# Kernel tuning notes

Hardware: AMD Instinct MI355X
Metric: run time of the kernel (lower is better)

The kernel has to match this reference:

```python
import jax, jax.numpy as jnp
import numpy as np

D = 1024; H = 16; K = 64; BK = 32; FFN = 4096; LORA = 48; CHUNK = 64
THETA_CLIP = float(np.pi / 2)
THETA_INIT = float(np.pi / 16)


def layernorm(x, g, b, eps=1e-6):
    m = x.mean(-1, keepdims=True)
    v = ((x - m) ** 2).mean(-1, keepdims=True)
    return (x - m) * jax.lax.rsqrt(v + eps) * g + b


def setup_inputs() -> dict:
    key = jax.random.key(0)
    ks = jax.random.split(key, 24)
    w = lambda k, s: jax.random.normal(k, s, jnp.float32) * 0.02
    return {
        "x": jax.random.normal(ks[0], (4, 2048, D), jnp.float32),
        "Wq": w(ks[1], (D, D)), "bq": jnp.zeros((D,), jnp.float32),
        "Wk": w(ks[2], (D, D)), "bk": jnp.zeros((D,), jnp.float32),
        "Wv": w(ks[3], (D, D)), "bv": jnp.zeros((D,), jnp.float32),
        "Wo": w(ks[4], (D, D)), "bo": jnp.zeros((D,), jnp.float32),
        "n1g": jnp.ones((D,), jnp.float32), "n1b": jnp.zeros((D,), jnp.float32),
        "n2g": jnp.ones((D,), jnp.float32), "n2b": jnp.zeros((D,), jnp.float32),
        "theta_base": jax.random.uniform(ks[5], (H, BK), jnp.float32, -THETA_INIT, THETA_INIT),
        "theta_w1": w(ks[6], (D, LORA)),
        "theta_w2": jax.random.uniform(ks[7], (LORA, H * BK), jnp.float32, -0.01, 0.01),
        "lambda_base": jax.random.uniform(ks[8], (H, BK), jnp.float32, 0.5, 6.0),
        "eta": jax.random.normal(ks[9], (H, BK), jnp.float32) * 0.1,
        "Wf1": w(ks[10], (D, FFN)), "bf1": jnp.zeros((FFN,), jnp.float32),
        "Wf2": w(ks[11], (FFN, D)), "bf2": jnp.zeros((D,), jnp.float32),
    }


def _forward(x, Wq, bq, Wk, bk, Wv, bv, Wo, bo, n1g, n1b, n2g, n2b,
             theta_base, theta_w1, theta_w2, lambda_base, eta, Wf1, bf1, Wf2, bf2):
    B, T, _ = x.shape
    NC = T // CHUNK
    xn = layernorm(x, n1g, n1b)
    # projections -> (B, H, T, K)
    q = (xn @ Wq + bq).reshape(B, T, H, K).transpose(0, 2, 1, 3)
    k = (xn @ Wk + bk).reshape(B, T, H, K).transpose(0, 2, 1, 3)
    v = (xn @ Wv + bv).reshape(B, T, H, K).transpose(0, 2, 1, 3)
    phi_k = jnp.where(k > 0, k + 1.0, jnp.exp(k))  # elu(k) + 1
    qp = q.reshape(B, H, T, BK, 2)
    kp = phi_k.reshape(B, H, T, BK, 2)
    q_c = jax.lax.complex(qp[..., 0], qp[..., 1])  # (B,H,T,BK) complex64
    k_c = jax.lax.complex(kp[..., 0], kp[..., 1])
    # data-dependent rotation angles via LoRA
    lora = jnp.tanh(xn @ theta_w1) @ theta_w2  # (B,T,H*BK)
    theta = theta_base[None, None] + lora.reshape(B, T, H, BK)
    theta = jnp.clip(theta, -THETA_CLIP, THETA_CLIP).transpose(0, 2, 1, 3)  # (B,H,T,BK)
    lam = lambda_base[None, :, None, :] + eta[None, :, None, :] * theta ** 2
    log_z = jax.lax.complex(-lam, theta)  # complex log-decay per step

    def chunks(a):  # (B,H,T,...) -> (NC,B,H,CHUNK,...)
        return jnp.moveaxis(a.reshape(B, H, NC, CHUNK, *a.shape[3:]), 2, 0)

    tril = jnp.tril(jnp.ones((CHUNK, CHUNK), bool))[None, None, :, :, None]

    def step(c, inputs):
        lz, kc, qc, vf = inputs  # (B,H,tc,BK)x3, (B,H,tc,K)
        cumlog = jnp.cumsum(lz, axis=2)
        diff = cumlog[:, :, :, None, :] - cumlog[:, :, None, :, :]  # (B,H,tc,tc,BK)
        real = jnp.where(tril, diff.real, -60.0)
        A = jnp.where(tril, jnp.exp(jax.lax.complex(real, diff.imag)),
                      jnp.zeros((), jnp.complex64))
        scaled_k = A * kc[:, :, None, :, :]
        S_intra = jnp.einsum('bhtsk,bhsv->bhtkv', scaled_k, vf.astype(jnp.complex64))
        decay = jnp.exp(cumlog)
        S_total = decay[..., None] * c[:, :, None] + S_intra  # (B,H,tc,BK,K)
        y = jnp.einsum('bhtk,bhtkv->bhtv', jnp.conj(qc), S_total).real
        return S_total[:, :, -1], y

    c0 = jnp.zeros((B, H, BK, K), jnp.complex64)
    _, ys = jax.lax.scan(step, c0, (chunks(log_z), chunks(k_c), chunks(q_c), chunks(v)))
    out = jnp.moveaxis(ys, 0, 2).reshape(B, H, T, K)
    attn = out.transpose(0, 2, 1, 3).reshape(B, T, D) @ Wo + bo
    x1 = x + attn
    h = layernorm(x1, n2g, n2b)
    return x1 + jax.nn.gelu(h @ Wf1 + bf1) @ Wf2 + bf2


def reference(x, Wq, bq, Wk, bk, Wv, bv, Wo, bo, n1g, n1b, n2g, n2b,
              theta_base, theta_w1, theta_w2, lambda_base, eta, Wf1, bf1, Wf2, bf2):
    return _forward(x, Wq, bq, Wk, bk, Wv, bv, Wo, bo, n1g, n1b, n2g, n2b,
                    theta_base, theta_w1, theta_w2, lambda_base, eta, Wf1, bf1, Wf2, bf2)
```

## Files before the change

### kernel.cpp

```cpp
#include <hip/hip_runtime.h>


typedef __bf16 bf16x8 __attribute__((ext_vector_type(8)));
typedef float f32x4 __attribute__((ext_vector_type(4)));

__device__ __forceinline__ unsigned short f2bf(float f) {
  unsigned int u = __builtin_bit_cast(unsigned int, f);
  u += 0x7FFFu + ((u >> 16) & 1u);
  return (unsigned short)(u >> 16);
}
__device__ __forceinline__ float bf2f(unsigned short u) {
  unsigned int x = ((unsigned int)u) << 16;
  return __builtin_bit_cast(float, x);
}
__device__ __forceinline__ unsigned int pack2(float a, float b) {
  return (unsigned int)f2bf(a) | ((unsigned int)f2bf(b) << 16);
}

__device__ __forceinline__ void gload_lds16(const void* g, void* l) {
  __builtin_amdgcn_global_load_lds((const __attribute__((address_space(1))) void*)g,
                                   (__attribute__((address_space(3))) void*)l, 16, 0, 0);
}

__device__ __forceinline__ float gelu_tanh(float v) {
  const float z = 0.7978845608028654f * fmaf(0.044715f * v * v, v, v);
  const float e = __expf(2.f * z);
  return 0.5f * v * (2.f - 2.f / (1.f + e));
}

__global__ void fill_kernel(float* p, float v, int n) {
  int i = blockIdx.x * 256 + threadIdx.x;
  if (i < n) p[i] = v;
}

__global__ __launch_bounds__(256) void ln_kernel(
    const float* __restrict__ x, const float* __restrict__ g,
    const float* __restrict__ b, unsigned short* __restrict__ out) {
  const int row = blockIdx.x, tid = threadIdx.x;
  float4 v = ((const float4*)(x + (size_t)row * 1024))[tid];
  float s = v.x + v.y + v.z + v.w;
  float sq = v.x * v.x + v.y * v.y + v.z * v.z + v.w * v.w;
#pragma unroll
  for (int o = 32; o > 0; o >>= 1) { s += __shfl_xor(s, o); sq += __shfl_xor(sq, o); }
  __shared__ float red[8];
  const int wid = tid >> 6;
  if ((tid & 63) == 0) { red[wid] = s; red[4 + wid] = sq; }
  __syncthreads();
  s = red[0] + red[1] + red[2] + red[3];
  sq = red[4] + red[5] + red[6] + red[7];
  const float mean = s * (1.f / 1024.f);
  const float var = sq * (1.f / 1024.f) - mean * mean;
  const float rstd = rsqrtf(var + 1e-6f);
  float4 gv = ((const float4*)g)[tid];
  float4 bvv = ((const float4*)b)[tid];
  ushort4 o4;
  o4.x = f2bf((v.x - mean) * rstd * gv.x + bvv.x);
  o4.y = f2bf((v.y - mean) * rstd * gv.y + bvv.y);
  o4.z = f2bf((v.z - mean) * rstd * gv.z + bvv.z);
  o4.w = f2bf((v.w - mean) * rstd * gv.w + bvv.w);
  *(ushort4*)(out + (size_t)row * 1024 + tid * 4) = o4;
}

__global__ __launch_bounds__(256) void transpose_bf16(
    const float* __restrict__ src, unsigned short* __restrict__ dst, int K, int N) {
  __shared__ float tile[32][33];
  const int n0 = blockIdx.x * 32, k0 = blockIdx.y * 32;
  const int tx = threadIdx.x, ty = threadIdx.y;
#pragma unroll
  for (int j = 0; j < 32; j += 8) tile[tx][ty + j] = src[(size_t)(k0 + ty + j) * N + n0 + tx];
  __syncthreads();
#pragma unroll
  for (int j = 0; j < 32; j += 8)
    dst[(size_t)(n0 + ty + j) * K + k0 + tx] = f2bf(tile[ty + j][tx]);
}

__global__ __launch_bounds__(256) void prep_wcat(
    const float* __restrict__ Wq, const float* __restrict__ Wk,
    const float* __restrict__ Wv, const float* __restrict__ tw1,
    unsigned short* __restrict__ dst) {
  __shared__ float tile[32][33];
  const int r0 = blockIdx.x * 32, c0 = blockIdx.y * 32;
  const int tx = threadIdx.x, ty = threadIdx.y;
  const int r = r0 + tx;
#pragma unroll
  for (int j = 0; j < 32; j += 8) {
    const int c = c0 + ty + j;
    float v;
    if (r < 1024) v = Wq[(size_t)c * 1024 + r];
    else if (r < 2048) v = Wk[(size_t)c * 1024 + (r - 1024)];
    else if (r < 3072) v = Wv[(size_t)c * 1024 + (r - 2048)];
    else if (r < 3120) v = tw1[(size_t)c * 48 + (r - 3072)];
    else v = 0.f;
    tile[tx][ty + j] = v;
  }
  __syncthreads();
#pragma unroll
  for (int j = 0; j < 32; j += 8)
    dst[(size_t)(r0 + ty + j) * 1024 + c0 + tx] = f2bf(tile[ty + j][tx]);
}

__global__ void biascat_kernel(const float* bq, const float* bk, const float* bv, float* dst) {
  int i = blockIdx.x * 256 + threadIdx.x;
  if (i >= 3200) return;
  float v = 0.f;
  if (i < 1024) v = bq[i];
  else if (i < 2048) v = bk[i - 1024];
  else if (i < 3072) v = bv[i - 2048];
  dst[i] = v;
}

template <int MODE>
__global__ __launch_bounds__(256) void gemm_kernel(
    const unsigned short* __restrict__ A, const unsigned short* __restrict__ BT,
    const float* __restrict__ bias, const float* __restrict__ res,
    void* __restrict__ out, int N, int Kd) {
  __shared__ unsigned short As[128 * 64];
  __shared__ unsigned short Bs[128 * 64];
  const int nwg = gridDim.x * gridDim.y;
  int d = blockIdx.y * gridDim.x + blockIdx.x;
  d = (d & 7) * (nwg >> 3) + (d >> 3);
  const int n0 = (d % gridDim.x) * 128, m0 = (d / gridDim.x) * 128;

  const int tid = threadIdx.x, wv = tid >> 6, ln = tid & 63;
  const int wm = wv >> 1, wn = wv & 1;
  const int l15 = ln & 15, hi4 = ln >> 4;
  const int rbase = wv * 8 + (ln >> 3);
  const int kgofs = ((ln & 7) ^ ((ln >> 3) & 7)) * 8;

  f32x4 acc[4][4] = {};
  for (int k0 = 0; k0 < Kd; k0 += 64) {
#pragma unroll
    for (int jj = 0; jj < 4; ++jj) {
      gload_lds16(A + (size_t)(m0 + jj * 32 + rbase) * Kd + k0 + kgofs,
                  (char*)As + (jj * 256 + wv * 64) * 16);
      gload_lds16(BT + (size_t)(n0 + jj * 32 + rbase) * Kd + k0 + kgofs,
                  (char*)Bs + (jj * 256 + wv * 64) * 16);
    }
    __syncthreads();
#pragma unroll
    for (int kk = 0; kk < 64; kk += 32) {
      const int kg = (kk >> 3) + hi4;
      bf16x8 av[4], bv[4];
#pragma unroll
      for (int f = 0; f < 4; ++f) {
        const int ra = wm * 64 + f * 16 + l15;
        const int rb2 = wn * 64 + f * 16 + l15;
        av[f] = *(const bf16x8*)&As[(ra * 8 + (kg ^ (ra & 7))) * 8];
        bv[f] = *(const bf16x8*)&Bs[(rb2 * 8 + (kg ^ (rb2 & 7))) * 8];
      }
#pragma unroll
      for (int fm = 0; fm < 4; ++fm)
#pragma unroll
        for (int fn = 0; fn < 4; ++fn)
          acc[fm][fn] = __builtin_amdgcn_mfma_f32_16x16x32_bf16(av[fm], bv[fn], acc[fm][fn], 0, 0, 0);
    }
    __syncthreads();
  }
  const int rb = hi4 * 4;
#pragma unroll
  for (int fm = 0; fm < 4; ++fm) {
#pragma unroll
    for (int fn = 0; fn < 4; ++fn) {
      const int row = m0 + wm * 64 + fm * 16 + rb;
      const int col = n0 + wn * 64 + fn * 16 + l15;
      const float bval = bias[col];
#pragma unroll
      for (int r = 0; r < 4; ++r) {
        float v = acc[fm][fn][r] + bval;
        const size_t oi = (size_t)(row + r) * N + col;
        if constexpr (MODE == 1) v += res[oi];
        if constexpr (MODE == 2) {
          ((unsigned short*)out)[oi] = f2bf(gelu_tanh(v));
        } else if constexpr (MODE == 3) {
          ((unsigned short*)out)[oi] = f2bf(v);
        } else {
          ((float*)out)[oi] = v;
        }
      }
    }
  }
}

__global__ __launch_bounds__(256) void lora2_kernel(
    const unsigned short* __restrict__ qkv, const float* __restrict__ w2,
    const float* __restrict__ tbase, float* __restrict__ theta) {
  __shared__ float lt[8][48];
  const int m0 = blockIdx.x * 32;
  const int tid = threadIdx.x;
  const int col = tid * 2;
  const float tb0 = tbase[col], tb1 = tbase[col + 1];
  for (int grp = 0; grp < 4; ++grp) {
    const int mg = m0 + grp * 8;
    __syncthreads();
    for (int idx = tid; idx < 384; idx += 256) {
      const int tok = idx / 48, jj = idx % 48;
      lt[tok][jj] = tanhf(bf2f(qkv[(size_t)(mg + tok) * 3200 + 3072 + jj]));
    }
    __syncthreads();
    float a0[8], a1[8];
#pragma unroll
    for (int tok = 0; tok < 8; ++tok) { a0[tok] = tb0; a1[tok] = tb1; }
    for (int jj = 0; jj < 48; ++jj) {
      const float2 w = *(const float2*)&w2[(size_t)jj * 512 + col];
#pragma unroll
      for (int tok = 0; tok < 8; ++tok) {
        const float l = lt[tok][jj];
        a0[tok] = fmaf(l, w.x, a0[tok]);
        a1[tok] = fmaf(l, w.y, a1[tok]);
      }
    }
    const float CL = 1.5707963267948966f;
#pragma unroll
    for (int tok = 0; tok < 8; ++tok) {
      float c0 = fminf(fmaxf(a0[tok], -CL), CL);
      float c1 = fminf(fmaxf(a1[tok], -CL), CL);
      *(float2*)&theta[(size_t)(mg + tok) * 512 + col] = make_float2(c0, c1);
    }
  }
}

__global__ __launch_bounds__(256) void attn_intra(
    const unsigned short* __restrict__ qkv, const float* __restrict__ theta,
    const float* __restrict__ lamb, const float* __restrict__ eta,
    float* __restrict__ yi, unsigned short* __restrict__ QG,
    unsigned short* __restrict__ TCG, float* __restrict__ Dg) {
  const int c = blockIdx.x, bh = blockIdx.y;
  const int b = bh >> 4, h = bh & 15;
  const int tid = threadIdx.x, wv = tid >> 6, lane = tid & 63;
  const int sc = c * 4 + wv;
  const int cid = bh * 128 + sc;
  const int mw = b * 2048 + sc * 16;

  __shared__ unsigned short QDm[4][16][64];
  __shared__ unsigned short KDm[4][16][64];
  __shared__ unsigned short KdET[4][64][32];
  __shared__ unsigned short VT[4][64][32];
  __shared__ unsigned short Gs[4][16][32];

  {
    unsigned int* kz = (unsigned int*)&KdET[wv][0][0];
    unsigned int* vz = (unsigned int*)&VT[wv][0][0];
    for (int idx = lane; idx < 512; idx += 64) {
      const int r = idx >> 3, p = (idx & 7) + 8;
      kz[r * 16 + p] = 0; vz[r * 16 + p] = 0;
    }
    unsigned int* gz = (unsigned int*)&Gs[wv][0][0];
    for (int idx = lane; idx < 128; idx += 64) {
      const int r = idx >> 3, p = (idx & 7) + 8;
      gz[r * 16 + p] = 0;
    }
  }
  for (int ss = 0; ss < 16; ++ss)
    VT[wv][lane][ss] = qkv[(size_t)(mw + ss) * 3200 + 2048 + h * 64 + lane];

  const int bk = lane & 31, th = lane >> 5;
  const float lb = lamb[h * 32 + bk], et = eta[h * 32 + bk];
  float L[8], Th[8], qr[8], qi[8], kr[8], ki[8];
  float runL = 0.f, runT = 0.f;
#pragma unroll
  for (int i = 0; i < 8; ++i) {
    const size_t m = (size_t)(mw + th * 8 + i);
    const float tv = theta[m * 512 + h * 32 + bk];
    const float lam = fmaf(et * tv, tv, lb);
    runL += lam; L[i] = runL;
    runT += tv;  Th[i] = runT;
    const unsigned int qp = *(const unsigned int*)&qkv[m * 3200 + h * 64 + 2 * bk];
    const unsigned int kp = *(const unsigned int*)&qkv[m * 3200 + 1024 + h * 64 + 2 * bk];
    qr[i] = bf2f((unsigned short)(qp & 0xFFFF)); qi[i] = bf2f((unsigned short)(qp >> 16));
    const float kx = bf2f((unsigned short)(kp & 0xFFFF));
    const float ky = bf2f((unsigned short)(kp >> 16));
    kr[i] = kx > 0.f ? kx + 1.f : __expf(kx);
    ki[i] = ky > 0.f ? ky + 1.f : __expf(ky);
  }
  const float oL = __shfl_xor(runL, 32), oT = __shfl_xor(runT, 32);
  const float Lm = th ? oL : runL;
  const float Tm = th ? oT : runT;
  const float Ltot = runL + oL, Ttot = runT + oT;
  const float Lbase = th ? oL : 0.f, Tbase = th ? oT : 0.f;
  float Es, Ec; __sincosf(Tm, &Es, &Ec);
  const float Ee = __expf(-Lm);
  const float Er = Ee * Ec, Ei = Ee * Es;
  float Fs, Fc; __sincosf(Ttot - Tm, &Fs, &Fc);
  const float Fe = __expf(-(Ltot - Lm));
  const float Fr = Fe * Fc, Fi = Fe * Fs;
  if (th == 0) {
    float Ds, Dc; __sincosf(Ttot, &Ds, &Dc);
    const float De = __expf(-Ltot);
    *(float2*)&Dg[((size_t)cid * 32 + bk) * 2] = make_float2(De * Dc, De * Ds);
  }
  unsigned int* qd32 = (unsigned int*)&QDm[wv][0][0];
  unsigned int* kd32 = (unsigned int*)&KDm[wv][0][0];
#pragma unroll
  for (int i = 0; i < 8; ++i) {
    const int t = th * 8 + i;
    const float Lg = Lbase + L[i], Tg = Tbase + Th[i];
    const float dm = __expf(-(Lg - Lm));
    float sn, cs; __sincosf(Tg - Tm, &sn, &cs);
    const float qmr = dm * (qr[i] * cs + qi[i] * sn);
    const float qmi = dm * (qr[i] * sn - qi[i] * cs);
    const float rd = 1.f / dm;
    const float kmr = rd * (kr[i] * cs + ki[i] * sn);
    const float kmi = rd * (ki[i] * cs - kr[i] * sn);
    const int sidx = (t * 32 + bk) ^ ((t & 7) << 2);
    qd32[sidx] = pack2(qmr, qmi);
    kd32[sidx] = pack2(kmr, -kmi);
    ((unsigned int*)QG)[(size_t)cid * 512 + t * 32 + bk] =
        pack2(qmr * Er - qmi * Ei, qmr * Ei + qmi * Er);
    const float er = kmr * Fr - kmi * Fi;
    const float ei = kmr * Fi + kmi * Fr;
    KdET[wv][bk][t] = f2bf(er);
    KdET[wv][32 + bk][t] = f2bf(ei);
  }

  const int l15 = lane & 15, hi = lane >> 4;
  const char* qb = (const char*)&QDm[wv][0][0];
  const char* kb = (const char*)&KDm[wv][0][0];
  f32x4 z = {};
  f32x4 g = z;
  {
    bf16x8 a0 = *(const bf16x8*)(qb + l15 * 128 + ((16 * hi) ^ ((l15 & 7) << 4)));
    bf16x8 b0 = *(const bf16x8*)(kb + l15 * 128 + ((16 * hi) ^ ((l15 & 7) << 4)));
    bf16x8 a1 = *(const bf16x8*)(qb + l15 * 128 + ((64 + 16 * hi) ^ ((l15 & 7) << 4)));
    bf16x8 b1 = *(const bf16x8*)(kb + l15 * 128 + ((64 + 16 * hi) ^ ((l15 & 7) << 4)));
    g = __builtin_amdgcn_mfma_f32_16x16x32_bf16(a0, b0, g, 0, 0, 0);
    g = __builtin_amdgcn_mfma_f32_16x16x32_bf16(a1, b1, g, 0, 0, 0);
  }
#pragma unroll
  for (int r = 0; r < 4; ++r) {
    const float gv = (l15 <= 4 * hi + r) ? g[r] : 0.f;
    Gs[wv][4 * hi + r][l15] = f2bf(gv);
  }
  const char* gsb = (const char*)&Gs[wv][0][0];
  const char* vtb = (const char*)&VT[wv][0][0];
  bf16x8 aG = *(const bf16x8*)(gsb + l15 * 64 + 16 * hi);
#pragma unroll
  for (int nt = 0; nt < 4; ++nt) {
    bf16x8 bV = *(const bf16x8*)(vtb + (nt * 16 + l15) * 64 + 16 * hi);
    f32x4 y = __builtin_amdgcn_mfma_f32_16x16x32_bf16(aG, bV, z, 0, 0, 0);
#pragma unroll
    for (int r = 0; r < 4; ++r)
      yi[(size_t)cid * 1024 + (4 * hi + r) * 64 + nt * 16 + l15] = y[r];
  }
  const char* keb = (const char*)&KdET[wv][0][0];
#pragma unroll
  for (int mt = 0; mt < 4; ++mt) {
    bf16x8 aT = *(const bf16x8*)(keb + (mt * 16 + l15) * 64 + 16 * hi);
#pragma unroll
    for (int nt = 0; nt < 4; ++nt) {
      bf16x8 bV = *(const bf16x8*)(vtb + (nt * 16 + l15) * 64 + 16 * hi);
      f32x4 t4 = __builtin_amdgcn_mfma_f32_16x16x32_bf16(aT, bV, z, 0, 0, 0);
#pragma unroll
      for (int r = 0; r < 4; ++r)
        TCG[(size_t)cid * 4096 + (mt * 16 + 4 * hi + r) * 64 + nt * 16 + l15] = f2bf(t4[r]);
    }
  }
}

__global__ __launch_bounds__(256) void scanB_kernel(
    const unsigned short* __restrict__ TCG, const float* __restrict__ Dg,
    unsigned int* __restrict__ CPACK) {
  const int bh = blockIdx.x & 63, g = blockIdx.x >> 6;
  const int tid = threadIdx.x;
  const int v = g * 8 + (tid >> 5), bk = tid & 31;
  const size_t base = (size_t)bh * 128;
  float Cr = 0.f, Ci = 0.f;
  float trx[4], tix[4]; float2 dx[4];
  auto LOADQ = [&](int c0, float* tr, float* ti, float2* dd) {
#pragma unroll
    for (int u = 0; u < 4; ++u) {
      const size_t cid = base + c0 + u;
      tr[u] = bf2f(TCG[cid * 4096 + bk * 64 + v]);
      ti[u] = bf2f(TCG[cid * 4096 + (32 + bk) * 64 + v]);
      dd[u] = *(const float2*)&Dg[(cid * 32 + bk) * 2];
    }
  };
  LOADQ(0, trx, tix, dx);
  for (int c0 = 0; c0 < 128; c0 += 4) {
    float tra[4], tia[4]; float2 da[4];
#pragma unroll
    for (int u = 0; u < 4; ++u) { tra[u] = trx[u]; tia[u] = tix[u]; da[u] = dx[u]; }
    if (c0 + 4 < 128) LOADQ(c0 + 4, trx, tix, dx);
#pragma unroll
    for (int u = 0; u < 4; ++u) {
      CPACK[(base + c0 + u) * 2048 + v * 32 + bk] = pack2(Cr, -Ci);
      const float nr = fmaf(da[u].x, Cr, fmaf(-da[u].y, Ci, tra[u]));
      const float ni = fmaf(da[u].x, Ci, fmaf(da[u].y, Cr, tia[u]));
      Cr = nr; Ci = ni;
    }
  }
}

__global__ __launch_bounds__(256) void attn_cross(
    const float* __restrict__ yi, const unsigned short* __restrict__ QG,
    const unsigned int* __restrict__ CPACK, unsigned short* __restrict__ attn) {
  const int c = blockIdx.x, bh = blockIdx.y;
  const int b = bh >> 4, h = bh & 15;
  const int tid = threadIdx.x, wv = tid >> 6, lane = tid & 63;
  const int sc = c * 4 + wv, cid = bh * 128 + sc;
  const int mw = b * 2048 + sc * 16;
  __shared__ unsigned short Cp[4][64][64];
  __shared__ unsigned short Qs[4][16][64];
  unsigned int* cp32 = (unsigned int*)&Cp[wv][0][0];
  const unsigned int* cg = CPACK + (size_t)cid * 2048;
  for (int ii = 0; ii < 32; ++ii) {
    const int flat = ii * 64 + lane;
    const int row = flat >> 5, col = flat & 31;
    cp32[(row * 32 + col) ^ ((row & 7) << 2)] = cg[flat];
  }
  unsigned int* qs32 = (unsigned int*)&Qs[wv][0][0];
  const unsigned int* qg = (const unsigned int*)QG + (size_t)cid * 512;
  for (int ii = 0; ii < 8; ++ii) {
    const int flat = ii * 64 + lane;
    const int row = flat >> 5, col = flat & 31;
    qs32[(row * 32 + col) ^ ((row & 7) << 2)] = qg[flat];
  }
  const int l15 = lane & 15, hi = lane >> 4;
  const char* qb = (const char*)&Qs[wv][0][0];
  const char* cb = (const char*)&Cp[wv][0][0];
  bf16x8 a0 = *(const bf16x8*)(qb + l15 * 128 + ((16 * hi) ^ ((l15 & 7) << 4)));
  bf16x8 a1 = *(const bf16x8*)(qb + l15 * 128 + ((64 + 16 * hi) ^ ((l15 & 7) << 4)));
  f32x4 z = {};
#pragma unroll
  for (int nt = 0; nt < 4; ++nt) {
    const int vr = nt * 16 + l15;
    bf16x8 b0 = *(const bf16x8*)(cb + vr * 128 + ((16 * hi) ^ ((vr & 7) << 4)));
    bf16x8 b1 = *(const bf16x8*)(cb + vr * 128 + ((64 + 16 * hi) ^ ((vr & 7) << 4)));
    f32x4 y = __builtin_amdgcn_mfma_f32_16x16x32_bf16(a0, b0, z, 0, 0, 0);
    y = __builtin_amdgcn_mfma_f32_16x16x32_bf16(a1, b1, y, 0, 0, 0);
#pragma unroll
    for (int r = 0; r < 4; ++r) {
      const int t = 4 * hi + r;
      const float out = y[r] + yi[(size_t)cid * 1024 + t * 64 + vr];
      attn[(size_t)(mw + t) * 1024 + h * 64 + vr] = f2bf(out);
    }
  }
}

extern "C" void kernel_launch(void* const* d_in, const int* in_sizes, int n_in,
                              void* d_out, int out_size, void* d_ws, size_t ws_size,
                              hipStream_t stream) {
  const float* x   = (const float*)d_in[0];
  const float* Wq  = (const float*)d_in[1];
  const float* bq  = (const float*)d_in[2];
  const float* Wk  = (const float*)d_in[3];
  const float* bk_ = (const float*)d_in[4];
  const float* Wv  = (const float*)d_in[5];
  const float* bv  = (const float*)d_in[6];
  const float* Wo  = (const float*)d_in[7];
  const float* bo  = (const float*)d_in[8];
  const float* n1g = (const float*)d_in[9];
  const float* n1b = (const float*)d_in[10];
  const float* n2g = (const float*)d_in[11];
  const float* n2b = (const float*)d_in[12];
  const float* thb = (const float*)d_in[13];
  const float* tw1 = (const float*)d_in[14];
  const float* tw2 = (const float*)d_in[15];
  const float* lamb= (const float*)d_in[16];
  const float* eta = (const float*)d_in[17];
  const float* Wf1 = (const float*)d_in[18];
  const float* bf1 = (const float*)d_in[19];
  const float* Wf2 = (const float*)d_in[20];
  const float* bf2 = (const float*)d_in[21];

  char* ws = (char*)d_ws;
  size_t off = 0;
  auto alloc = [&](size_t bytes) {
    size_t r = off;
    off += (bytes + 255) & ~(size_t)255;
    return r;
  };
  unsigned short* WCAT = (unsigned short*)(ws + alloc(3200ull * 1024 * 2));
  unsigned short* WOT  = (unsigned short*)(ws + alloc(1024ull * 1024 * 2));
  unsigned short* WF1T = (unsigned short*)(ws + alloc(4096ull * 1024 * 2));
  unsigned short* WF2T = (unsigned short*)(ws + alloc(1024ull * 4096 * 2));
  float* BIASC = (float*)(ws + alloc(3200ull * 4));
  unsigned short* XN = (unsigned short*)(ws + alloc(8192ull * 1024 * 2));
  char* QKVbase = ws + alloc(8192ull * 4096 * 2);
  unsigned short* QKV = (unsigned short*)QKVbase;
  unsigned int* CPACK = (unsigned int*)QKVbase;
  unsigned short* GBUF = (unsigned short*)QKVbase;
  float* THETA = (float*)(ws + alloc(8192ull * 512 * 4));
  unsigned short* ATTN = (unsigned short*)THETA;
  float* YI = (float*)(ws + alloc(8192ull * 1024 * 4));
  float* X1 = YI;
  unsigned short* QG = (unsigned short*)(ws + alloc(8192ull * 1024 * 2));
  unsigned short* TCG = (unsigned short*)(ws + alloc(8192ull * 4096 * 2));
  float* DG = (float*)(ws + alloc(8192ull * 32 * 2 * 4));

  if (ws_size < off) {
    fill_kernel<<<dim3((out_size + 255) / 256), dim3(256), 0, stream>>>((float*)d_out, 12345.0f, out_size);
    return;
  }

  const dim3 b256(256), b32x8(32, 8);

  prep_wcat<<<dim3(100, 32), b32x8, 0, stream>>>(Wq, Wk, Wv, tw1, WCAT);
  transpose_bf16<<<dim3(32, 32), b32x8, 0, stream>>>(Wo, WOT, 1024, 1024);
  transpose_bf16<<<dim3(128, 32), b32x8, 0, stream>>>(Wf1, WF1T, 1024, 4096);
  transpose_bf16<<<dim3(32, 128), b32x8, 0, stream>>>(Wf2, WF2T, 4096, 1024);
  biascat_kernel<<<dim3(13), b256, 0, stream>>>(bq, bk_, bv, BIASC);

  ln_kernel<<<dim3(8192), b256, 0, stream>>>(x, n1g, n1b, XN);
  gemm_kernel<3><<<dim3(25, 64), b256, 0, stream>>>(XN, WCAT, BIASC, nullptr, QKV, 3200, 1024);
  lora2_kernel<<<dim3(256), b256, 0, stream>>>(QKV, tw2, thb, THETA);
  attn_intra<<<dim3(32, 64), b256, 0, stream>>>(QKV, THETA, lamb, eta, YI, QG, TCG, DG);
  scanB_kernel<<<dim3(512), b256, 0, stream>>>(TCG, DG, CPACK);
  attn_cross<<<dim3(32, 64), b256, 0, stream>>>(YI, QG, CPACK, ATTN);
  gemm_kernel<1><<<dim3(8, 64), b256, 0, stream>>>(ATTN, WOT, bo, x, X1, 1024, 1024);
  ln_kernel<<<dim3(8192), b256, 0, stream>>>(X1, n2g, n2b, XN);
  gemm_kernel<2><<<dim3(32, 64), b256, 0, stream>>>(XN, WF1T, bf1, nullptr, GBUF, 4096, 1024);
  gemm_kernel<1><<<dim3(8, 64), b256, 0, stream>>>(GBUF, WF2T, bf2, X1, d_out, 1024, 4096);
}
```

Measured before the change: 520.9 us.

## Replace GEMM with double-buffered 512-thread kernel, fuse prep launches, retile scan output layout

Swaps the single-buffered 128x128 GEMM for a 512-thread kernel that double-buffers A/B tiles in LDS with K-step 32, uses explicit vmcnt waits and barriers, raises MFMA priority, and optionally processes 256-row M tiles. The goal is to overlap global loads with MFMA work and get more reuse per block. It also merges the weight transpose and bias concat kernels into one launch, pads the QKV width to 3328, and changes the CPACK layout so scan writes and cross-attention reads are coalesced. The hand-written waitcnt pipeline is fragile, and the padding adds some wasted GEMM columns.

```diff
diff --git a/kernel.cpp b/kernel.cpp
--- a/kernel.cpp
+++ b/kernel.cpp
@@ -1,5 +1,7 @@
 #include <hip/hip_runtime.h>
 
+
+#define QS 3328
 
 typedef __bf16 bf16x8 __attribute__((ext_vector_type(8)));
 typedef float f32x4 __attribute__((ext_vector_type(4)));
@@ -61,11 +63,11 @@
   *(ushort4*)(out + (size_t)row * 1024 + tid * 4) = o4;
 }
 
-__global__ __launch_bounds__(256) void transpose_bf16(
-    const float* __restrict__ src, unsigned short* __restrict__ dst, int K, int N) {
+__device__ __forceinline__ void tr_tile(
+    const float* __restrict__ src, unsigned short* __restrict__ dst,
+    int K, int N, int bx, int by, int tx, int ty) {
   __shared__ float tile[32][33];
-  const int n0 = blockIdx.x * 32, k0 = blockIdx.y * 32;
-  const int tx = threadIdx.x, ty = threadIdx.y;
+  const int n0 = bx * 32, k0 = by * 32;
 #pragma unroll
   for (int j = 0; j < 32; j += 8) tile[tx][ty + j] = src[(size_t)(k0 + ty + j) * N + n0 + tx];
   __syncthreads();
@@ -74,107 +76,165 @@
     dst[(size_t)(n0 + ty + j) * K + k0 + tx] = f2bf(tile[ty + j][tx]);
 }
 
-__global__ __launch_bounds__(256) void prep_wcat(
+__global__ __launch_bounds__(256) void prep_all(
     const float* __restrict__ Wq, const float* __restrict__ Wk,
     const float* __restrict__ Wv, const float* __restrict__ tw1,
-    unsigned short* __restrict__ dst) {
-  __shared__ float tile[32][33];
-  const int r0 = blockIdx.x * 32, c0 = blockIdx.y * 32;
-  const int tx = threadIdx.x, ty = threadIdx.y;
-  const int r = r0 + tx;
-#pragma unroll
-  for (int j = 0; j < 32; j += 8) {
-    const int c = c0 + ty + j;
-    float v;
-    if (r < 1024) v = Wq[(size_t)c * 1024 + r];
-    else if (r < 2048) v = Wk[(size_t)c * 1024 + (r - 1024)];
-    else if (r < 3072) v = Wv[(size_t)c * 1024 + (r - 2048)];
-    else if (r < 3120) v = tw1[(size_t)c * 48 + (r - 3072)];
-    else v = 0.f;
-    tile[tx][ty + j] = v;
-  }
-  __syncthreads();
-#pragma unroll
-  for (int j = 0; j < 32; j += 8)
-    dst[(size_t)(r0 + ty + j) * 1024 + c0 + tx] = f2bf(tile[ty + j][tx]);
-}
-
-__global__ void biascat_kernel(const float* bq, const float* bk, const float* bv, float* dst) {
-  int i = blockIdx.x * 256 + threadIdx.x;
-  if (i >= 3200) return;
-  float v = 0.f;
-  if (i < 1024) v = bq[i];
-  else if (i < 2048) v = bk[i - 1024];
-  else if (i < 3072) v = bv[i - 2048];
-  dst[i] = v;
-}
-
-template <int MODE>
-__global__ __launch_bounds__(256) void gemm_kernel(
+    const float* __restrict__ Wo, const float* __restrict__ Wf1,
+    const float* __restrict__ Wf2,
+    const float* __restrict__ bq, const float* __restrict__ bk,
+    const float* __restrict__ bv,
+    unsigned short* __restrict__ WCAT, unsigned short* __restrict__ WOT,
+    unsigned short* __restrict__ WF1T, unsigned short* __restrict__ WF2T,
+    float* __restrict__ BIASC) {
+  const int id = blockIdx.x;
+  const int tx = threadIdx.x & 31, ty = threadIdx.x >> 5;
+  if (id < 3328) {
+    __shared__ float tile[32][33];
+    const int bx = id % 104, by = id / 104;
+    const int r0 = bx * 32, c0 = by * 32;
+    const int r = r0 + tx;
+#pragma unroll
+    for (int j = 0; j < 32; j += 8) {
+      const int c = c0 + ty + j;
+      float v;
+      if (r < 1024) v = Wq[(size_t)c * 1024 + r];
+      else if (r < 2048) v = Wk[(size_t)c * 1024 + (r - 1024)];
+      else if (r < 3072) v = Wv[(size_t)c * 1024 + (r - 2048)];
+      else if (r < 3120) v = tw1[(size_t)c * 48 + (r - 3072)];
+      else v = 0.f;
+      tile[tx][ty + j] = v;
+    }
+    __syncthreads();
+#pragma unroll
+    for (int j = 0; j < 32; j += 8)
+      WCAT[(size_t)(r0 + ty + j) * 1024 + c0 + tx] = f2bf(tile[ty + j][tx]);
+  } else if (id < 4352) {
+    const int i2 = id - 3328;
+    tr_tile(Wo, WOT, 1024, 1024, i2 % 32, i2 / 32, tx, ty);
+  } else if (id < 8448) {
+    const int i3 = id - 4352;
+    tr_tile(Wf1, WF1T, 1024, 4096, i3 % 128, i3 / 128, tx, ty);
+  } else if (id < 12544) {
+    const int i4 = id - 8448;
+    tr_tile(Wf2, WF2T, 4096, 1024, i4 % 32, i4 / 32, tx, ty);
+  } else {
+    const int i5 = (id - 12544) * 256 + threadIdx.x;
+    if (i5 < QS) {
+      float v = 0.f;
+      if (i5 < 1024) v = bq[i5];
+      else if (i5 < 2048) v = bk[i5 - 1024];
+      else if (i5 < 3072) v = bv[i5 - 2048];
+      BIASC[i5] = v;
+    }
+  }
+}
+
+template <int MODE, int MB>
+__global__ __launch_bounds__(512, 4) void gemmco_kernel(
     const unsigned short* __restrict__ A, const unsigned short* __restrict__ BT,
     const float* __restrict__ bias, const float* __restrict__ res,
-    void* __restrict__ out, int N, int Kd) {
-  __shared__ unsigned short As[128 * 64];
-  __shared__ unsigned short Bs[128 * 64];
+    void* __restrict__ out, int N, int Kstride, int Klen) {
+  constexpr int NR = (MB == 2) ? 4 : 2;
+  constexpr int ABUF = MB * 8192;
+  __shared__ __align__(16) char SA[2 * ABUF];
+  __shared__ __align__(16) char SB[2 * 8192];
+
   const int nwg = gridDim.x * gridDim.y;
   int d = blockIdx.y * gridDim.x + blockIdx.x;
   d = (d & 7) * (nwg >> 3) + (d >> 3);
-  const int n0 = (d % gridDim.x) * 128, m0 = (d / gridDim.x) * 128;
+  const int n0 = (d % gridDim.x) * 128, m0 = (d / gridDim.x) * (MB * 128);
 
   const int tid = threadIdx.x, wv = tid >> 6, ln = tid & 63;
-  const int wm = wv >> 1, wn = wv & 1;
-  const int l15 = ln & 15, hi4 = ln >> 4;
-  const int rbase = wv * 8 + (ln >> 3);
-  const int kgofs = ((ln & 7) ^ ((ln >> 3) & 7)) * 8;
-
-  f32x4 acc[4][4] = {};
-  for (int k0 = 0; k0 < Kd; k0 += 64) {
-#pragma unroll
-    for (int jj = 0; jj < 4; ++jj) {
-      gload_lds16(A + (size_t)(m0 + jj * 32 + rbase) * Kd + k0 + kgofs,
-                  (char*)As + (jj * 256 + wv * 64) * 16);
-      gload_lds16(BT + (size_t)(n0 + jj * 32 + rbase) * Kd + k0 + kgofs,
-                  (char*)Bs + (jj * 256 + wv * 64) * 16);
-    }
-    __syncthreads();
-#pragma unroll
-    for (int kk = 0; kk < 64; kk += 32) {
-      const int kg = (kk >> 3) + hi4;
-      bf16x8 av[4], bv[4];
-#pragma unroll
-      for (int f = 0; f < 4; ++f) {
-        const int ra = wm * 64 + f * 16 + l15;
-        const int rb2 = wn * 64 + f * 16 + l15;
-        av[f] = *(const bf16x8*)&As[(ra * 8 + (kg ^ (ra & 7))) * 8];
-        bv[f] = *(const bf16x8*)&Bs[(rb2 * 8 + (kg ^ (rb2 & 7))) * 8];
-      }
-#pragma unroll
-      for (int fm = 0; fm < 4; ++fm)
-#pragma unroll
-        for (int fn = 0; fn < 4; ++fn)
-          acc[fm][fn] = __builtin_amdgcn_mfma_f32_16x16x32_bf16(av[fm], bv[fn], acc[fm][fn], 0, 0, 0);
-    }
-    __syncthreads();
-  }
-  const int rb = hi4 * 4;
-#pragma unroll
-  for (int fm = 0; fm < 4; ++fm) {
-#pragma unroll
-    for (int fn = 0; fn < 4; ++fn) {
-      const int row = m0 + wm * 64 + fm * 16 + rb;
-      const int col = n0 + wn * 64 + fn * 16 + l15;
+  const int l15 = ln & 15, hi4 = (ln >> 4) & 3;
+  const int wm = (MB == 2) ? (wv >> 1) : (wv >> 2);
+  const int wncol = (MB == 2) ? (wv & 1) * 64 : (wv & 3) * 32;
+
+  const int srow = ln >> 2;
+  const int skg = (ln & 3) ^ ((ln >> 3) & 3);
+  const unsigned short* ga0 = A + (size_t)(m0 + wv * 16 + srow) * Kstride + skg * 8;
+  const unsigned short* ga1 = A + (size_t)(m0 + 128 + wv * 16 + srow) * Kstride + skg * 8;
+  const unsigned short* gb0 = BT + (size_t)(n0 + wv * 16 + srow) * Kstride + skg * 8;
+
+  auto STA = [&](int p) {
+    gload_lds16(ga0, SA + p * ABUF + wv * 1024);
+    ga0 += 32;
+    if constexpr (MB == 2) {
+      gload_lds16(ga1, SA + p * ABUF + 8192 + wv * 1024);
+      ga1 += 32;
+    }
+  };
+  auto STB = [&](int p) {
+    gload_lds16(gb0, SB + p * 8192 + wv * 1024);
+    gb0 += 32;
+  };
+
+  const int kch = (hi4 ^ ((l15 >> 1) & 3)) * 16;
+  const char* aA = SA + (wm * 64 + l15) * 64 + kch;
+  const char* aB = SB + (wncol + l15) * 64 + kch;
+
+  f32x4 acc[4][NR] = {};
+  const int nt = Klen >> 5;
+
+  STA(0);
+  STB(0);
+  STA(1);
+  if constexpr (MB == 2) asm volatile("s_waitcnt vmcnt(2)" ::: "memory");
+  else                   asm volatile("s_waitcnt vmcnt(1)" ::: "memory");
+  __builtin_amdgcn_s_barrier();
+
+#define GTILE(P, T)                                                            \
+  {                                                                            \
+    if ((T) + 1 < nt) STB((P) ^ 1);                                            \
+    bf16x8 bfr[NR];                                                            \
+    _Pragma("unroll")                                                          \
+    for (int nr = 0; nr < NR; ++nr)                                            \
+      bfr[nr] = *(const bf16x8*)(aB + (P) * 8192 + nr * 1024);                 \
+    _Pragma("unroll")                                                          \
+    for (int mr = 0; mr < 4; ++mr) {                                           \
+      bf16x8 af = *(const bf16x8*)(aA + (P) * ABUF + mr * 1024);               \
+      __builtin_amdgcn_s_setprio(1);                                           \
+      _Pragma("unroll")                                                        \
+      for (int nr = 0; nr < NR; ++nr)                                          \
+        acc[mr][nr] = __builtin_amdgcn_mfma_f32_16x16x32_bf16(af, bfr[nr],     \
+                                                              acc[mr][nr], 0, 0, 0); \
+      __builtin_amdgcn_s_setprio(0);                                           \
+    }                                                                          \
+    __builtin_amdgcn_s_barrier();                                              \
+    if ((T) + 2 < nt) STA(P);                                                  \
+    if ((T) + 1 < nt) {                                                        \
+      if ((T) + 2 < nt) {                                                      \
+        if constexpr (MB == 2) asm volatile("s_waitcnt vmcnt(2)" ::: "memory");\
+        else                   asm volatile("s_waitcnt vmcnt(1)" ::: "memory");\
+      } else {                                                                 \
+        asm volatile("s_waitcnt vmcnt(0)" ::: "memory");                       \
+      }                                                                        \
+      __builtin_amdgcn_s_barrier();                                            \
+    }                                                                          \
+  }
+
+  for (int t = 0; t < nt; t += 2) {
+    GTILE(0, t);
+    GTILE(1, t + 1);
+  }
+#undef GTILE
+
+#pragma unroll
+  for (int mr = 0; mr < 4; ++mr) {
+#pragma unroll
+    for (int nr = 0; nr < NR; ++nr) {
+      const int row = m0 + wm * 64 + mr * 16 + hi4 * 4;
+      const int col = n0 + wncol + nr * 16 + l15;
       const float bval = bias[col];
 #pragma unroll
       for (int r = 0; r < 4; ++r) {
-        float v = acc[fm][fn][r] + bval;
+        const float v = acc[mr][nr][r] + bval;
         const size_t oi = (size_t)(row + r) * N + col;
-        if constexpr (MODE == 1) v += res[oi];
-        if constexpr (MODE == 2) {
+        if constexpr (MODE == 1) {
+          ((float*)out)[oi] = v + res[oi];
+        } else if constexpr (MODE == 2) {
           ((unsigned short*)out)[oi] = f2bf(gelu_tanh(v));
-        } else if constexpr (MODE == 3) {
+        } else {
           ((unsigned short*)out)[oi] = f2bf(v);
-        } else {
-          ((float*)out)[oi] = v;
         }
       }
     }
@@ -194,7 +254,7 @@
     __syncthreads();
     for (int idx = tid; idx < 384; idx += 256) {
       const int tok = idx / 48, jj = idx % 48;
-      lt[tok][jj] = tanhf(bf2f(qkv[(size_t)(mg + tok) * 3200 + 3072 + jj]));
+      lt[tok][jj] = tanhf(bf2f(qkv[(size_t)(mg + tok) * QS + 3072 + jj]));
     }
     __syncthreads();
     float a0[8], a1[8];
@@ -251,7 +311,7 @@
     }
   }
   for (int ss = 0; ss < 16; ++ss)
-    VT[wv][lane][ss] = qkv[(size_t)(mw + ss) * 3200 + 2048 + h * 64 + lane];
+    VT[wv][lane][ss] = qkv[(size_t)(mw + ss) * QS + 2048 + h * 64 + lane];
 
   const int bk = lane & 31, th = lane >> 5;
   const float lb = lamb[h * 32 + bk], et = eta[h * 32 + bk];
@@ -264,8 +324,8 @@
     const float lam = fmaf(et * tv, tv, lb);
     runL += lam; L[i] = runL;
     runT += tv;  Th[i] = runT;
-    const unsigned int qp = *(const unsigned int*)&qkv[m * 3200 + h * 64 + 2 * bk];
-    const unsigned int kp = *(const unsigned int*)&qkv[m * 3200 + 1024 + h * 64 + 2 * bk];
+    const unsigned int qp = *(const unsigned int*)&qkv[m * QS + h * 64 + 2 * bk];
+    const unsigned int kp = *(const unsigned int*)&qkv[m * QS + 1024 + h * 64 + 2 * bk];
     qr[i] = bf2f((unsigned short)(qp & 0xFFFF)); qi[i] = bf2f((unsigned short)(qp >> 16));
     const float kx = bf2f((unsigned short)(kp & 0xFFFF));
     const float ky = bf2f((unsigned short)(kp >> 16));
@@ -361,7 +421,7 @@
     unsigned int* __restrict__ CPACK) {
   const int bh = blockIdx.x & 63, g = blockIdx.x >> 6;
   const int tid = threadIdx.x;
-  const int v = g * 8 + (tid >> 5), bk = tid & 31;
+  const int v = tid & 63, bk = g * 4 + (tid >> 6);
   const size_t base = (size_t)bh * 128;
   float Cr = 0.f, Ci = 0.f;
   float trx[4], tix[4]; float2 dx[4];
@@ -382,7 +442,7 @@
     if (c0 + 4 < 128) LOADQ(c0 + 4, trx, tix, dx);
 #pragma unroll
     for (int u = 0; u < 4; ++u) {
-      CPACK[(base + c0 + u) * 2048 + v * 32 + bk] = pack2(Cr, -Ci);
+      CPACK[(base + c0 + u) * 2048 + bk * 64 + v] = pack2(Cr, -Ci);
       const float nr = fmaf(da[u].x, Cr, fmaf(-da[u].y, Ci, tra[u]));
       const float ni = fmaf(da[u].x, Ci, fmaf(da[u].y, Cr, tia[u]));
       Cr = nr; Ci = ni;
@@ -402,10 +462,8 @@
   __shared__ unsigned short Qs[4][16][64];
   unsigned int* cp32 = (unsigned int*)&Cp[wv][0][0];
   const unsigned int* cg = CPACK + (size_t)cid * 2048;
-  for (int ii = 0; ii < 32; ++ii) {
-    const int flat = ii * 64 + lane;
-    const int row = flat >> 5, col = flat & 31;
-    cp32[(row * 32 + col) ^ ((row & 7) << 2)] = cg[flat];
+  for (int bkq = 0; bkq < 32; ++bkq) {
+    cp32[(lane * 32 + bkq) ^ ((lane & 7) << 2)] = cg[bkq * 64 + lane];
   }
   unsigned int* qs32 = (unsigned int*)&Qs[wv][0][0];
   const unsigned int* qg = (const unsigned int*)QG + (size_t)cid * 512;
@@ -469,11 +527,11 @@
     off += (bytes + 255) & ~(size_t)255;
     return r;
   };
-  unsigned short* WCAT = (unsigned short*)(ws + alloc(3200ull * 1024 * 2));
+  unsigned short* WCAT = (unsigned short*)(ws + alloc((size_t)QS * 1024 * 2));
   unsigned short* WOT  = (unsigned short*)(ws + alloc(1024ull * 1024 * 2));
   unsigned short* WF1T = (unsigned short*)(ws + alloc(4096ull * 1024 * 2));
   unsigned short* WF2T = (unsigned short*)(ws + alloc(1024ull * 4096 * 2));
-  float* BIASC = (float*)(ws + alloc(3200ull * 4));
+  float* BIASC = (float*)(ws + alloc((size_t)QS * 4));
   unsigned short* XN = (unsigned short*)(ws + alloc(8192ull * 1024 * 2));
   char* QKVbase = ws + alloc(8192ull * 4096 * 2);
   unsigned short* QKV = (unsigned short*)QKVbase;
@@ -492,22 +550,19 @@
     return;
   }
 
-  const dim3 b256(256), b32x8(32, 8);
-
-  prep_wcat<<<dim3(100, 32), b32x8, 0, stream>>>(Wq, Wk, Wv, tw1, WCAT);
-  transpose_bf16<<<dim3(32, 32), b32x8, 0, stream>>>(Wo, WOT, 1024, 1024);
-  transpose_bf16<<<dim3(128, 32), b32x8, 0, stream>>>(Wf1, WF1T, 1024, 4096);
-  transpose_bf16<<<dim3(32, 128), b32x8, 0, stream>>>(Wf2, WF2T, 4096, 1024);
-  biascat_kernel<<<dim3(13), b256, 0, stream>>>(bq, bk_, bv, BIASC);
+  const dim3 b256(256), b512(512);
+
+  prep_all<<<dim3(12557), b256, 0, stream>>>(Wq, Wk, Wv, tw1, Wo, Wf1, Wf2,
+                                             bq, bk_, bv, WCAT, WOT, WF1T, WF2T, BIASC);
 
   ln_kernel<<<dim3(8192), b256, 0, stream>>>(x, n1g, n1b, XN);
-  gemm_kernel<3><<<dim3(25, 64), b256, 0, stream>>>(XN, WCAT, BIASC, nullptr, QKV, 3200, 1024);
+  gemmco_kernel<3, 2><<<dim3(26, 32), b512, 0, stream>>>(XN, WCAT, BIASC, nullptr, QKV, QS, 1024, 1024);
   lora2_kernel<<<dim3(256), b256, 0, stream>>>(QKV, tw2, thb, THETA);
   attn_intra<<<dim3(32, 64), b256, 0, stream>>>(QKV, THETA, lamb, eta, YI, QG, TCG, DG);
   scanB_kernel<<<dim3(512), b256, 0, stream>>>(TCG, DG, CPACK);
   attn_cross<<<dim3(32, 64), b256, 0, stream>>>(YI, QG, CPACK, ATTN);
-  gemm_kernel<1><<<dim3(8, 64), b256, 0, stream>>>(ATTN, WOT, bo, x, X1, 1024, 1024);
+  gemmco_kernel<1, 1><<<dim3(8, 64), b512, 0, stream>>>(ATTN, WOT, bo, x, X1, 1024, 1024, 1024);
   ln_kernel<<<dim3(8192), b256, 0, stream>>>(X1, n2g, n2b, XN);
-  gemm_kernel<2><<<dim3(32, 64), b256, 0, stream>>>(XN, WF1T, bf1, nullptr, GBUF, 4096, 1024);
-  gemm_kernel<1><<<dim3(8, 64), b256, 0, stream>>>(GBUF, WF2T, bf2, X1, d_out, 1024, 4096);
-}
+  gemmco_kernel<2, 2><<<dim3(32, 32), b512, 0, stream>>>(XN, WF1T, bf1, nullptr, GBUF, 4096, 1024, 1024);
+  gemmco_kernel<1, 1><<<dim3(8, 64), b512, 0, stream>>>(GBUF, WF2T, bf2, X1, (float*)d_out, 1024, 4096, 4096);
+}
```

Measured after the change: 437.5 us. 16.0% less time.
